# Performance work log

Hardware: AMD Instinct MI355X
Metric: run time of the kernel (lower is better)

Reference implementation:

```python
import jax, jax.numpy as jnp
import numpy as np

E = 768   # embed_size
H = 64    # head_embed_size
B = 8
T = 4096  # == ctx_size


def setup_inputs() -> dict:
    key = jax.random.key(0)
    k1, k2, k3, k4 = jax.random.split(key, 4)
    inputs = jax.random.normal(k1, (B, T, E), dtype=jnp.float32)
    # Linear weights stored as (E, H) so projection is x @ W
    scale = 1.0 / np.sqrt(E)
    Wq = jax.random.uniform(k2, (E, H), dtype=jnp.float32, minval=-scale, maxval=scale)
    Wk = jax.random.uniform(k3, (E, H), dtype=jnp.float32, minval=-scale, maxval=scale)
    Wv = jax.random.uniform(k4, (E, H), dtype=jnp.float32, minval=-scale, maxval=scale)
    return {"inputs": inputs, "Wq": Wq, "Wk": Wk, "Wv": Wv}


def reference(inputs, Wq, Wk, Wv):
    Tlen = inputs.shape[1]
    q = inputs @ Wq  # (B,T,H)
    k = inputs @ Wk  # (B,T,H)
    v = inputs @ Wv  # (B,T,H)
    # NOTE: original module does NOT scale by 1/sqrt(H) — faithful reproduction.
    scores = jnp.einsum('bqh,bkh->bqk', q, k)  # (B,T,T)
    causal = jnp.tril(jnp.ones((Tlen, Tlen), dtype=bool))
    scores = jnp.where(causal, scores, -jnp.inf)
    attn = jax.nn.softmax(scores, axis=-1)
    # dropout=0 -> identity
    out = jnp.einsum('bqk,bkh->bqh', attn, v)  # (B,T,H)
    return out
```

## Files before the change

kernel.cpp:

```cpp
#include <hip/hip_runtime.h>
#include <hip/hip_bf16.h>

#define E_DIM 768
#define H_DIM 64
#define B_SZ 8
#define T_SZ 4096
#define BT (B_SZ * T_SZ)

typedef __attribute__((ext_vector_type(8))) short short8;
typedef __attribute__((ext_vector_type(4))) short bf16x4;
typedef __attribute__((ext_vector_type(4))) float floatx4;

#define RAWBAR() __asm__ volatile("s_waitcnt lgkmcnt(0)\n\ts_barrier" ::: "memory")

static __device__ __forceinline__ unsigned short bf1(float a) {
    __hip_bfloat16 h = __float2bfloat16(a);
    unsigned short u; __builtin_memcpy(&u, &h, 2); return u;
}
static __device__ __forceinline__ unsigned int pk2(float a, float b) {
    __hip_bfloat162 h = __float22bfloat162_rn(float2{a, b});
    unsigned int u; __builtin_memcpy(&u, &h, 4); return u;
}

__global__ __launch_bounds__(256) void prep_w(
    const float* __restrict__ Wq, const float* __restrict__ Wk,
    const float* __restrict__ Wv, unsigned short* __restrict__ Wt)
{
    __shared__ float Ls[64][65];
    const int nt = blockIdx.x;
    const int kc = blockIdx.y;
    const float* __restrict__ W = (nt == 0) ? Wq : (nt == 1) ? Wk : Wv;
    const float scl = (nt == 0) ? 1.44269504088896f : 1.0f;
    const int t = threadIdx.x;
    const int k0 = kc * 64;

#pragma unroll
    for (int it = 0; it < 16; ++it) {
        const int kk = (t >> 6) + it * 4;
        Ls[kk][t & 63] = W[(size_t)(k0 + kk) * H_DIM + (t & 63)];
    }
    __syncthreads();

#pragma unroll
    for (int it = 0; it < 4; ++it) {
        const int nl = (t >> 4) + it * 16;
        const int kl = (t & 15) * 4;
        unsigned int u[2];
        u[0] = pk2(Ls[kl + 0][nl] * scl, Ls[kl + 1][nl] * scl);
        u[1] = pk2(Ls[kl + 2][nl] * scl, Ls[kl + 3][nl] * scl);
        *(uint2*)(Wt + (size_t)(nt * 64 + nl) * E_DIM + k0 + kl) = *(uint2*)u;
    }
}

__global__ __launch_bounds__(768) void proj_mfma(
    const float* __restrict__ X, const unsigned short* __restrict__ Wt,
    unsigned short* __restrict__ Qb, unsigned short* __restrict__ Kb,
    unsigned short* __restrict__ Vtb)
{
    __shared__ unsigned short Xs[2][16][776];

    const int tid  = threadIdx.x;
    const int wave = tid >> 6, lane = tid & 63;
    const int row  = lane & 15, quad = lane >> 4;
    const int m0   = blockIdx.x * 128;

    short8 bfr[24];
    {
        const unsigned short* wp = Wt + (size_t)(wave * 16 + row) * E_DIM + quad * 8;
#pragma unroll
        for (int ks = 0; ks < 24; ++ks) bfr[ks] = *(const short8*)(wp + ks * 32);
    }

    const int srow = tid & 15;
    const int sc   = tid >> 4;
    const float* __restrict__ xbase = X + (size_t)(m0 + srow) * E_DIM + sc * 16;

    float4 fx[4];
#define LDX(mt)                                                               \
    {                                                                         \
        const float* p = xbase + (size_t)(mt) * 16 * E_DIM;                   \
        fx[0] = *(const float4*)(p);     fx[1] = *(const float4*)(p + 4);     \
        fx[2] = *(const float4*)(p + 8); fx[3] = *(const float4*)(p + 12);    \
    }
#define STX(buf)                                                              \
    {                                                                         \
        unsigned int tmp[8];                                                  \
        tmp[0] = pk2(fx[0].x, fx[0].y); tmp[1] = pk2(fx[0].z, fx[0].w);       \
        tmp[2] = pk2(fx[1].x, fx[1].y); tmp[3] = pk2(fx[1].z, fx[1].w);       \
        tmp[4] = pk2(fx[2].x, fx[2].y); tmp[5] = pk2(fx[2].z, fx[2].w);       \
        tmp[6] = pk2(fx[3].x, fx[3].y); tmp[7] = pk2(fx[3].z, fx[3].w);       \
        *(int4*)&Xs[buf][srow][sc * 16]     = *(int4*)&tmp[0];                \
        *(int4*)&Xs[buf][srow][sc * 16 + 8] = *(int4*)&tmp[4];                \
    }

    LDX(0); STX(0); LDX(1);
    RAWBAR();

    const int g  = wave >> 2;
    const int h  = (wave & 3) * 16 + row;
    unsigned short* __restrict__ OQK = (g == 0) ? Qb : Kb;
    const int bb = m0 >> 12;

    int cur = 0;
    for (int mt = 0; mt < 8; ++mt) {
        if (mt < 7) STX(cur ^ 1);
        if (mt < 6) LDX(mt + 2);

        floatx4 a0 = (floatx4)0.0f, a1 = (floatx4)0.0f;
        floatx4 a2 = (floatx4)0.0f, a3 = (floatx4)0.0f;
#pragma unroll
        for (int ks = 0; ks < 6; ++ks) {
            const short8 f0 = *(const short8*)&Xs[cur][row][(ks * 4 + 0) * 32 + quad * 8];
            const short8 f1 = *(const short8*)&Xs[cur][row][(ks * 4 + 1) * 32 + quad * 8];
            const short8 f2 = *(const short8*)&Xs[cur][row][(ks * 4 + 2) * 32 + quad * 8];
            const short8 f3 = *(const short8*)&Xs[cur][row][(ks * 4 + 3) * 32 + quad * 8];
            a0 = __builtin_amdgcn_mfma_f32_16x16x32_bf16(f0, bfr[ks * 4 + 0], a0, 0, 0, 0);
            a1 = __builtin_amdgcn_mfma_f32_16x16x32_bf16(f1, bfr[ks * 4 + 1], a1, 0, 0, 0);
            a2 = __builtin_amdgcn_mfma_f32_16x16x32_bf16(f2, bfr[ks * 4 + 2], a2, 0, 0, 0);
            a3 = __builtin_amdgcn_mfma_f32_16x16x32_bf16(f3, bfr[ks * 4 + 3], a3, 0, 0, 0);
        }
        floatx4 acc;
#pragma unroll
        for (int r = 0; r < 4; ++r) acc[r] = (a0[r] + a1[r]) + (a2[r] + a3[r]);

        const int mr = m0 + mt * 16 + quad * 4;
        if (g < 2) {
#pragma unroll
            for (int r = 0; r < 4; ++r)
                OQK[(size_t)(mr + r) * H_DIM + h] = bf1(acc[r]);
        } else {
            const int t0 = mr & 4095;
            unsigned int u[2];
            u[0] = pk2(acc[0], acc[1]); u[1] = pk2(acc[2], acc[3]);
            *(uint2*)(Vtb + ((size_t)bb * H_DIM + h) * T_SZ + t0) = *(uint2*)u;
        }

        RAWBAR();
        cur ^= 1;
    }
#undef LDX
#undef STX
}

__global__ __launch_bounds__(128, 6) void attn_mfma(
    const unsigned short* __restrict__ Qb,
    const unsigned short* __restrict__ Kb,
    const unsigned short* __restrict__ Vtb,
    float* __restrict__ Opart, float* __restrict__ lpart,
    float* __restrict__ Out)
{
    __shared__ __align__(16) unsigned short Ks[32][72];
    __shared__ __align__(16) unsigned short Vs[64][40];

    const int lb = blockIdx.x;
    const int b  = lb & 7;
    const int s  = lb >> 3;
    int qq, c, m;
    if (s < 48)       { m = 6; qq = 127 - s / 6;                      c = s % 6; }
    else if (s < 168) { m = 5; const int i = s - 48;  qq = 119 - i / 5;  c = i % 5; }
    else if (s < 264) { m = 4; const int i = s - 168; qq = 95 - (i >> 2); c = i & 3; }
    else if (s < 336) { m = 3; const int i = s - 264; qq = 71 - i / 3;   c = i % 3; }
    else if (s < 384) { m = 2; const int i = s - 336; qq = 47 - (i >> 1); c = i & 1; }
    else              { m = 1; qq = 407 - s; c = 0; }
    const int ntot = qq + 1;
    const int k0t  = (c * ntot) / m;
    const int k1t  = ((c + 1) * ntot) / m;
    const int ktd  = ntot - 1;
    const int n    = k1t - k0t;
    const bool split = (m > 1);

    const int tid  = threadIdx.x;
    const int wq   = tid >> 6;
    const int lane = tid & 63;
    const int col  = lane & 15, quad = lane >> 4;

    const size_t base = (size_t)b * T_SZ * H_DIM;
    const int q0  = qq * 32;

    short8 qf0, qf1;
    {
        const unsigned short* qp = Qb + base + (size_t)(q0 + wq * 16 + col) * H_DIM + quad * 8;
        qf0 = *(const short8*)(qp);
        qf1 = *(const short8*)(qp + 32);
    }

    floatx4 o[4];
#pragma unroll
    for (int i = 0; i < 4; ++i) o[i] = (floatx4)0.0f;
    float lp = 0.0f;

    const int krow = tid >> 2, kcol = (tid & 3) * 16;
    const int vrow = tid >> 1, vcol = (tid & 1) * 16;
    const unsigned short* __restrict__ Ksrc = Kb + base + (size_t)krow * H_DIM + kcol;
    const unsigned short* __restrict__ Vsrc = Vtb + ((size_t)b * H_DIM + vrow) * T_SZ + vcol;

    int4 kr0, kr1, vr0, vr1;
#define LDKV(t)                                                          \
    {                                                                    \
        const unsigned short* kp = Ksrc + (size_t)(t) * 32 * H_DIM;      \
        kr0 = *(const int4*)kp; kr1 = *(const int4*)(kp + 8);            \
        const unsigned short* vp = Vsrc + (t) * 32;                      \
        vr0 = *(const int4*)vp; vr1 = *(const int4*)(vp + 8);            \
    }
#define STKV()                                                           \
    {                                                                    \
        *(int4*)&Ks[krow][kcol] = kr0; *(int4*)&Ks[krow][kcol + 8] = kr1; \
        *(int4*)&Vs[vrow][vcol] = vr0; *(int4*)&Vs[vrow][vcol + 8] = vr1; \
    }

    LDKV(k0t);
    STKV();
    if (n > 1) LDKV(k0t + 1);
    RAWBAR();

    for (int i = 0; i < n; ++i) {
        const int kt = k0t + i;

        floatx4 sv[2];
        __builtin_amdgcn_s_setprio(1);
#pragma unroll
        for (int j = 0; j < 2; ++j) {
            const unsigned short* kp = &Ks[j * 16 + col][quad * 8];
            floatx4 a = (floatx4)0.0f;
            a = __builtin_amdgcn_mfma_f32_16x16x32_bf16(*(const short8*)(kp),      qf0, a, 0, 0, 0);
            a = __builtin_amdgcn_mfma_f32_16x16x32_bf16(*(const short8*)(kp + 32), qf1, a, 0, 0, 0);
            sv[j] = a;
        }
        __builtin_amdgcn_s_setprio(0);

        if (kt == ktd) {
            const int qg = q0 + wq * 16 + col;
#pragma unroll
            for (int j = 0; j < 2; ++j) {
                const int kb0 = kt * 32 + j * 16 + quad * 4;
#pragma unroll
                for (int r = 0; r < 4; ++r)
                    if (kb0 + r > qg) sv[j][r] = -1e30f;
            }
        }

        bf16x4 pa[2];
#pragma unroll
        for (int j = 0; j < 2; ++j) {
            float p0 = exp2f(sv[j][0]);
            float p1 = exp2f(sv[j][1]);
            float p2 = exp2f(sv[j][2]);
            float p3 = exp2f(sv[j][3]);
            lp += (p0 + p1) + (p2 + p3);
            unsigned int u0, u1;
            __asm__("v_cvt_pk_bf16_f32 %0, %1, %2" : "=v"(u0) : "v"(p0), "v"(p1));
            __asm__("v_cvt_pk_bf16_f32 %0, %1, %2" : "=v"(u1) : "v"(p2), "v"(p3));
            union { unsigned int u[2]; bf16x4 v; } pu;
            pu.u[0] = u0; pu.u[1] = u1;
            pa[j] = pu.v;
        }

        __builtin_amdgcn_s_setprio(1);
#pragma unroll
        for (int d = 0; d < 4; ++d) {
#pragma unroll
            for (int j = 0; j < 2; ++j) {
                const bf16x4 vb = *(const bf16x4*)(&Vs[d * 16 + col][j * 16 + quad * 4]);
                o[d] = __builtin_amdgcn_mfma_f32_16x16x16bf16_1k(pa[j], vb, o[d], 0, 0, 0);
            }
        }
        __builtin_amdgcn_s_setprio(0);

        RAWBAR();
        if (i + 1 < n) {
            STKV();
            if (i + 2 < n) LDKV(kt + 2);
        }
        RAWBAR();
    }

    lp += __shfl_xor(lp, 16);
    lp += __shfl_xor(lp, 32);
    float lr[4];
#pragma unroll
    for (int r = 0; r < 4; ++r) lr[r] = __shfl(lp, quad * 4 + r);

    if (!split) {
        float* op = Out + base + (size_t)(q0 + wq * 16 + quad * 4) * H_DIM;
#pragma unroll
        for (int r = 0; r < 4; ++r) {
            const float inv = 1.0f / lr[r];
#pragma unroll
            for (int d = 0; d < 4; ++d)
                op[(size_t)r * H_DIM + d * 16 + col] = o[d][r] * inv;
        }
    } else {
        const int pidx = (b * 128 + qq) * 6 + c;
        float* op = Opart + ((size_t)pidx * 32 + wq * 16 + quad * 4) * 64;
#pragma unroll
        for (int r = 0; r < 4; ++r)
#pragma unroll
            for (int d = 0; d < 4; ++d)
                op[(size_t)r * 64 + d * 16 + col] = o[d][r];
        if (quad == 0) lpart[pidx * 32 + wq * 16 + col] = lp;
    }
#undef LDKV
#undef STKV
}

__global__ __launch_bounds__(256) void attn_combine(
    const float* __restrict__ Opart, const float* __restrict__ lpart,
    float* __restrict__ Out)
{
    const int qq  = 24 + blockIdx.x;
    const int b   = blockIdx.y;
    const int m   = (qq + 24) / 24;
    const int tid = threadIdx.x;
    const int orow = tid >> 3;
    const int d0   = (tid & 7) * 8;
    const int p0   = (b * 128 + qq) * 6;

    float4 a0 = {0.f, 0.f, 0.f, 0.f}, a1 = {0.f, 0.f, 0.f, 0.f};
    float l = 0.0f;
    for (int j = 0; j < m; ++j) {
        const float* P = Opart + ((size_t)(p0 + j) * 32 + orow) * 64 + d0;
        const float4 b0 = *(const float4*)(P);
        const float4 b1 = *(const float4*)(P + 4);
        a0.x += b0.x; a0.y += b0.y; a0.z += b0.z; a0.w += b0.w;
        a1.x += b1.x; a1.y += b1.y; a1.z += b1.z; a1.w += b1.w;
        l += lpart[(p0 + j) * 32 + orow];
    }
    const float inv = 1.0f / l;
    a0.x *= inv; a0.y *= inv; a0.z *= inv; a0.w *= inv;
    a1.x *= inv; a1.y *= inv; a1.z *= inv; a1.w *= inv;

    float* op = Out + ((size_t)b * T_SZ + qq * 32 + orow) * H_DIM + d0;
    *(float4*)(op)     = a0;
    *(float4*)(op + 4) = a1;
}

extern "C" void kernel_launch(void* const* d_in, const int* in_sizes, int n_in,
                              void* d_out, int out_size, void* d_ws, size_t ws_size,
                              hipStream_t stream) {
    const float* X  = (const float*)d_in[0];
    const float* Wq = (const float*)d_in[1];
    const float* Wk = (const float*)d_in[2];
    const float* Wv = (const float*)d_in[3];

    unsigned short* Wt  = (unsigned short*)d_ws;
    unsigned short* Qb  = Wt + (size_t)192 * E_DIM;
    unsigned short* Kb  = Qb + (size_t)BT * H_DIM;
    unsigned short* Vtb = Kb + (size_t)BT * H_DIM;
    float* Opart = (float*)(Vtb + (size_t)BT * H_DIM);
    float* lpart = Opart + (size_t)6144 * 32 * 64;

    prep_w<<<dim3(3, 12), 256, 0, stream>>>(Wq, Wk, Wv, Wt);
    proj_mfma<<<256, 768, 0, stream>>>(X, Wt, Qb, Kb, Vtb);
    attn_mfma<<<3264, 128, 0, stream>>>(Qb, Kb, Vtb, Opart, lpart, (float*)d_out);
    attn_combine<<<dim3(104, 8), 256, 0, stream>>>(Opart, lpart, (float*)d_out);
}
```

Before: 222.8 us.

## Store K/V in MFMA fragment order and run LDS-free per-wave attention

The projection kernel now writes K and V directly in a pre-swizzled fragment layout, so each lane of the attention kernel can load its MFMA operands straight from global memory with contiguous 16-byte loads. Shared memory staging and barriers are removed. Each wave now handles 32 query rows independently, with register double-buffered K prefetch over 64-key steps. PV uses the 16x16x32 instruction, and the split-K schedule is rebalanced up to 8 chunks. The cost is more register pressure, and K/V are no longer shared across waves through LDS, so L2 traffic rises.

```diff
diff --git a/kernel.cpp b/kernel.cpp
--- a/kernel.cpp
+++ b/kernel.cpp
@@ -8,7 +8,6 @@
 #define BT (B_SZ * T_SZ)
 
 typedef __attribute__((ext_vector_type(8))) short short8;
-typedef __attribute__((ext_vector_type(4))) short bf16x4;
 typedef __attribute__((ext_vector_type(4))) float floatx4;
 
 #define RAWBAR() __asm__ volatile("s_waitcnt lgkmcnt(0)\n\ts_barrier" ::: "memory")
@@ -54,8 +53,8 @@
 
 __global__ __launch_bounds__(768) void proj_mfma(
     const float* __restrict__ X, const unsigned short* __restrict__ Wt,
-    unsigned short* __restrict__ Qb, unsigned short* __restrict__ Kb,
-    unsigned short* __restrict__ Vtb)
+    unsigned short* __restrict__ Qb, unsigned short* __restrict__ KFp,
+    unsigned short* __restrict__ VFp)
 {
     __shared__ unsigned short Xs[2][16][776];
 
@@ -98,7 +97,6 @@
 
     const int g  = wave >> 2;
     const int h  = (wave & 3) * 16 + row;
-    unsigned short* __restrict__ OQK = (g == 0) ? Qb : Kb;
     const int bb = m0 >> 12;
 
     int cur = 0;
@@ -124,15 +122,33 @@
         for (int r = 0; r < 4; ++r) acc[r] = (a0[r] + a1[r]) + (a2[r] + a3[r]);
 
         const int mr = m0 + mt * 16 + quad * 4;
-        if (g < 2) {
+        const int tl = mr & 4095;
+        if (g == 0) {
 #pragma unroll
             for (int r = 0; r < 4; ++r)
-                OQK[(size_t)(mr + r) * H_DIM + h] = bf1(acc[r]);
+                Qb[(size_t)(mr + r) * H_DIM + h] = bf1(acc[r]);
+        } else if (g == 1) {
+            const int kt = tl >> 6, kk = tl & 63;
+            const int j  = kk >> 5, rr = kk & 31;
+            const int gd = (rr >> 2) & 1;
+            const int C  = (rr >> 3) * 4;
+            const int qd = (h >> 3) & 3, fd = h >> 5, ed = h & 7;
+            unsigned short* kf = KFp +
+                ((((size_t)(bb * 64 + kt) * 2 + j) * 2 + gd) * 2 + fd) * 512 +
+                (qd * 16 + C) * 8 + ed;
+#pragma unroll
+            for (int r = 0; r < 4; ++r) kf[r * 8] = bf1(acc[r]);
         } else {
-            const int t0 = mr & 4095;
+            const int kt = tl >> 6, kk = tl & 63;
+            const int j  = kk >> 5, rr = kk & 31;
+            const int qv = rr >> 3, E = rr & 7;
+            const int d  = h >> 4, cv = h & 15;
             unsigned int u[2];
             u[0] = pk2(acc[0], acc[1]); u[1] = pk2(acc[2], acc[3]);
-            *(uint2*)(Vtb + ((size_t)bb * H_DIM + h) * T_SZ + t0) = *(uint2*)u;
+            unsigned short* vf = VFp +
+                (((size_t)(bb * 64 + kt) * 2 + j) * 4 + d) * 512 +
+                (qv * 16 + cv) * 8 + E;
+            *(uint2*)vf = *(uint2*)u;
         }
 
         RAWBAR();
@@ -142,183 +158,214 @@
 #undef STX
 }
 
-__global__ __launch_bounds__(128, 6) void attn_mfma(
+__global__ __launch_bounds__(256, 4) void attn_mfma(
     const unsigned short* __restrict__ Qb,
-    const unsigned short* __restrict__ Kb,
-    const unsigned short* __restrict__ Vtb,
+    const unsigned short* __restrict__ KF,
+    const unsigned short* __restrict__ VF,
     float* __restrict__ Opart, float* __restrict__ lpart,
     float* __restrict__ Out)
 {
-    __shared__ __align__(16) unsigned short Ks[32][72];
-    __shared__ __align__(16) unsigned short Vs[64][40];
-
     const int lb = blockIdx.x;
     const int b  = lb & 7;
-    const int s  = lb >> 3;
+    const int w  = threadIdx.x >> 6;
+    const int s  = (lb >> 3) * 4 + w;
     int qq, c, m;
-    if (s < 48)       { m = 6; qq = 127 - s / 6;                      c = s % 6; }
-    else if (s < 168) { m = 5; const int i = s - 48;  qq = 119 - i / 5;  c = i % 5; }
-    else if (s < 264) { m = 4; const int i = s - 168; qq = 95 - (i >> 2); c = i & 3; }
-    else if (s < 336) { m = 3; const int i = s - 264; qq = 71 - i / 3;   c = i % 3; }
-    else if (s < 384) { m = 2; const int i = s - 336; qq = 47 - (i >> 1); c = i & 1; }
-    else              { m = 1; qq = 407 - s; c = 0; }
-    const int ntot = qq + 1;
+    if (s < 128)      { m = 8; qq = 112 + (s >> 3);                  c = s & 7; }
+    else if (s < 240) { m = 7; const int i = s - 128; qq = 96 + i / 7; c = i % 7; }
+    else if (s < 336) { m = 6; const int i = s - 240; qq = 80 + i / 6; c = i % 6; }
+    else if (s < 416) { m = 5; const int i = s - 336; qq = 64 + i / 5; c = i % 5; }
+    else if (s < 480) { m = 4; const int i = s - 416; qq = 48 + (i >> 2); c = i & 3; }
+    else if (s < 528) { m = 3; const int i = s - 480; qq = 32 + i / 3; c = i % 3; }
+    else if (s < 560) { m = 2; const int i = s - 528; qq = 16 + (i >> 1); c = i & 1; }
+    else              { m = 1; qq = s - 560; c = 0; }
+    const int ntot = (qq >> 1) + 1;
     const int k0t  = (c * ntot) / m;
     const int k1t  = ((c + 1) * ntot) / m;
     const int ktd  = ntot - 1;
-    const int n    = k1t - k0t;
+    const int ns   = (k1t - k0t) * 2;
     const bool split = (m > 1);
 
-    const int tid  = threadIdx.x;
-    const int wq   = tid >> 6;
-    const int lane = tid & 63;
+    const int lane = threadIdx.x & 63;
     const int col  = lane & 15, quad = lane >> 4;
-
     const size_t base = (size_t)b * T_SZ * H_DIM;
-    const int q0  = qq * 32;
-
-    short8 qf0, qf1;
+    const int q0 = qq * 32;
+
+    short8 qfA0, qfA1, qfB0, qfB1;
     {
-        const unsigned short* qp = Qb + base + (size_t)(q0 + wq * 16 + col) * H_DIM + quad * 8;
-        qf0 = *(const short8*)(qp);
-        qf1 = *(const short8*)(qp + 32);
-    }
-
-    floatx4 o[4];
-#pragma unroll
-    for (int i = 0; i < 4; ++i) o[i] = (floatx4)0.0f;
-    float lp = 0.0f;
-
-    const int krow = tid >> 2, kcol = (tid & 3) * 16;
-    const int vrow = tid >> 1, vcol = (tid & 1) * 16;
-    const unsigned short* __restrict__ Ksrc = Kb + base + (size_t)krow * H_DIM + kcol;
-    const unsigned short* __restrict__ Vsrc = Vtb + ((size_t)b * H_DIM + vrow) * T_SZ + vcol;
-
-    int4 kr0, kr1, vr0, vr1;
-#define LDKV(t)                                                          \
-    {                                                                    \
-        const unsigned short* kp = Ksrc + (size_t)(t) * 32 * H_DIM;      \
-        kr0 = *(const int4*)kp; kr1 = *(const int4*)(kp + 8);            \
-        const unsigned short* vp = Vsrc + (t) * 32;                      \
-        vr0 = *(const int4*)vp; vr1 = *(const int4*)(vp + 8);            \
-    }
-#define STKV()                                                           \
-    {                                                                    \
-        *(int4*)&Ks[krow][kcol] = kr0; *(int4*)&Ks[krow][kcol + 8] = kr1; \
-        *(int4*)&Vs[vrow][vcol] = vr0; *(int4*)&Vs[vrow][vcol + 8] = vr1; \
-    }
-
-    LDKV(k0t);
-    STKV();
-    if (n > 1) LDKV(k0t + 1);
-    RAWBAR();
-
-    for (int i = 0; i < n; ++i) {
-        const int kt = k0t + i;
-
-        floatx4 sv[2];
-        __builtin_amdgcn_s_setprio(1);
-#pragma unroll
-        for (int j = 0; j < 2; ++j) {
-            const unsigned short* kp = &Ks[j * 16 + col][quad * 8];
-            floatx4 a = (floatx4)0.0f;
-            a = __builtin_amdgcn_mfma_f32_16x16x32_bf16(*(const short8*)(kp),      qf0, a, 0, 0, 0);
-            a = __builtin_amdgcn_mfma_f32_16x16x32_bf16(*(const short8*)(kp + 32), qf1, a, 0, 0, 0);
-            sv[j] = a;
-        }
-        __builtin_amdgcn_s_setprio(0);
-
-        if (kt == ktd) {
-            const int qg = q0 + wq * 16 + col;
-#pragma unroll
-            for (int j = 0; j < 2; ++j) {
-                const int kb0 = kt * 32 + j * 16 + quad * 4;
-#pragma unroll
-                for (int r = 0; r < 4; ++r)
-                    if (kb0 + r > qg) sv[j][r] = -1e30f;
+        const unsigned short* qp = Qb + base + (size_t)(q0 + col) * H_DIM + quad * 8;
+        qfA0 = *(const short8*)(qp);
+        qfA1 = *(const short8*)(qp + 32);
+        qfB0 = *(const short8*)(qp + 16 * H_DIM);
+        qfB1 = *(const short8*)(qp + 16 * H_DIM + 32);
+    }
+
+    floatx4 oA[4], oB[4];
+#pragma unroll
+    for (int i = 0; i < 4; ++i) { oA[i] = (floatx4)0.0f; oB[i] = (floatx4)0.0f; }
+    float lpA = 0.0f, lpB = 0.0f;
+
+    const unsigned short* __restrict__ KFb = KF + (size_t)b * 64 * 4096;
+    const unsigned short* __restrict__ VFb = VF + (size_t)b * 64 * 4096;
+    const int lo = lane * 8;
+
+    short8 kP0, kP1, kP2, kP3, kQ0, kQ1, kQ2, kQ3, v0, v1, v2, v3;
+
+#define LDK(S, ss_)                                                           \
+    {                                                                         \
+        const unsigned short* kp = KFb + (size_t)(k0t * 2 + (ss_)) * 2048 + lo; \
+        k##S##0 = *(const short8*)(kp);        k##S##1 = *(const short8*)(kp + 512);  \
+        k##S##2 = *(const short8*)(kp + 1024); k##S##3 = *(const short8*)(kp + 1536); \
+    }
+#define LDV(ss_)                                                              \
+    {                                                                         \
+        const unsigned short* vp = VFb + (size_t)(k0t * 2 + (ss_)) * 2048 + lo; \
+        v0 = *(const short8*)(vp);        v1 = *(const short8*)(vp + 512);    \
+        v2 = *(const short8*)(vp + 1024); v3 = *(const short8*)(vp + 1536);   \
+    }
+#define COMP(S, ss_)                                                          \
+    {                                                                         \
+        const int dia = ((ss_) >> 1) + k0t == ktd;                            \
+        floatx4 aA0 = (floatx4)0.0f, aA1 = (floatx4)0.0f;                     \
+        __builtin_amdgcn_s_setprio(1);                                        \
+        aA0 = __builtin_amdgcn_mfma_f32_16x16x32_bf16(k##S##0, qfA0, aA0, 0, 0, 0); \
+        aA1 = __builtin_amdgcn_mfma_f32_16x16x32_bf16(k##S##2, qfA0, aA1, 0, 0, 0); \
+        aA0 = __builtin_amdgcn_mfma_f32_16x16x32_bf16(k##S##1, qfA1, aA0, 0, 0, 0); \
+        aA1 = __builtin_amdgcn_mfma_f32_16x16x32_bf16(k##S##3, qfA1, aA1, 0, 0, 0); \
+        __builtin_amdgcn_s_setprio(0);                                        \
+        if (dia) {                                                            \
+            const int kb = ktd * 64 + ((ss_) & 1) * 32 + quad * 8;            \
+            const int qgA = q0 + col;                                         \
+            _Pragma("unroll")                                                 \
+            for (int r = 0; r < 4; ++r) {                                     \
+                if (kb + r > qgA)     aA0[r] = -1e30f;                        \
+                if (kb + 4 + r > qgA) aA1[r] = -1e30f;                        \
+            }                                                                 \
+        }                                                                     \
+        const float pA0 = exp2f(aA0[0]), pA1 = exp2f(aA0[1]);                 \
+        const float pA2 = exp2f(aA0[2]), pA3 = exp2f(aA0[3]);                 \
+        const float pA4 = exp2f(aA1[0]), pA5 = exp2f(aA1[1]);                 \
+        const float pA6 = exp2f(aA1[2]), pA7 = exp2f(aA1[3]);                 \
+        lpA += ((pA0 + pA1) + (pA2 + pA3)) + ((pA4 + pA5) + (pA6 + pA7));     \
+        unsigned int uA0, uA1, uA2, uA3;                                      \
+        __asm__("v_cvt_pk_bf16_f32 %0, %1, %2" : "=v"(uA0) : "v"(pA0), "v"(pA1)); \
+        __asm__("v_cvt_pk_bf16_f32 %0, %1, %2" : "=v"(uA1) : "v"(pA2), "v"(pA3)); \
+        __asm__("v_cvt_pk_bf16_f32 %0, %1, %2" : "=v"(uA2) : "v"(pA4), "v"(pA5)); \
+        __asm__("v_cvt_pk_bf16_f32 %0, %1, %2" : "=v"(uA3) : "v"(pA6), "v"(pA7)); \
+        union { unsigned int u[4]; short8 v; } puA;                           \
+        puA.u[0] = uA0; puA.u[1] = uA1; puA.u[2] = uA2; puA.u[3] = uA3;       \
+        const short8 paA = puA.v;                                             \
+        floatx4 aB0 = (floatx4)0.0f, aB1 = (floatx4)0.0f;                     \
+        __builtin_amdgcn_s_setprio(1);                                        \
+        aB0 = __builtin_amdgcn_mfma_f32_16x16x32_bf16(k##S##0, qfB0, aB0, 0, 0, 0); \
+        aB1 = __builtin_amdgcn_mfma_f32_16x16x32_bf16(k##S##2, qfB0, aB1, 0, 0, 0); \
+        aB0 = __builtin_amdgcn_mfma_f32_16x16x32_bf16(k##S##1, qfB1, aB0, 0, 0, 0); \
+        aB1 = __builtin_amdgcn_mfma_f32_16x16x32_bf16(k##S##3, qfB1, aB1, 0, 0, 0); \
+        __builtin_amdgcn_s_setprio(0);                                        \
+        if (dia) {                                                            \
+            const int kb = ktd * 64 + ((ss_) & 1) * 32 + quad * 8;            \
+            const int qgB = q0 + 16 + col;                                    \
+            _Pragma("unroll")                                                 \
+            for (int r = 0; r < 4; ++r) {                                     \
+                if (kb + r > qgB)     aB0[r] = -1e30f;                        \
+                if (kb + 4 + r > qgB) aB1[r] = -1e30f;                        \
+            }                                                                 \
+        }                                                                     \
+        const float pB0 = exp2f(aB0[0]), pB1 = exp2f(aB0[1]);                 \
+        const float pB2 = exp2f(aB0[2]), pB3 = exp2f(aB0[3]);                 \
+        const float pB4 = exp2f(aB1[0]), pB5 = exp2f(aB1[1]);                 \
+        const float pB6 = exp2f(aB1[2]), pB7 = exp2f(aB1[3]);                 \
+        lpB += ((pB0 + pB1) + (pB2 + pB3)) + ((pB4 + pB5) + (pB6 + pB7));     \
+        unsigned int uB0, uB1, uB2, uB3;                                      \
+        __asm__("v_cvt_pk_bf16_f32 %0, %1, %2" : "=v"(uB0) : "v"(pB0), "v"(pB1)); \
+        __asm__("v_cvt_pk_bf16_f32 %0, %1, %2" : "=v"(uB1) : "v"(pB2), "v"(pB3)); \
+        __asm__("v_cvt_pk_bf16_f32 %0, %1, %2" : "=v"(uB2) : "v"(pB4), "v"(pB5)); \
+        __asm__("v_cvt_pk_bf16_f32 %0, %1, %2" : "=v"(uB3) : "v"(pB6), "v"(pB7)); \
+        union { unsigned int u[4]; short8 v; } puB;                           \
+        puB.u[0] = uB0; puB.u[1] = uB1; puB.u[2] = uB2; puB.u[3] = uB3;       \
+        const short8 paB = puB.v;                                             \
+        __builtin_amdgcn_s_setprio(1);                                        \
+        oA[0] = __builtin_amdgcn_mfma_f32_16x16x32_bf16(paA, v0, oA[0], 0, 0, 0); \
+        oB[0] = __builtin_amdgcn_mfma_f32_16x16x32_bf16(paB, v0, oB[0], 0, 0, 0); \
+        oA[1] = __builtin_amdgcn_mfma_f32_16x16x32_bf16(paA, v1, oA[1], 0, 0, 0); \
+        oB[1] = __builtin_amdgcn_mfma_f32_16x16x32_bf16(paB, v1, oB[1], 0, 0, 0); \
+        oA[2] = __builtin_amdgcn_mfma_f32_16x16x32_bf16(paA, v2, oA[2], 0, 0, 0); \
+        oB[2] = __builtin_amdgcn_mfma_f32_16x16x32_bf16(paB, v2, oB[2], 0, 0, 0); \
+        oA[3] = __builtin_amdgcn_mfma_f32_16x16x32_bf16(paA, v3, oA[3], 0, 0, 0); \
+        oB[3] = __builtin_amdgcn_mfma_f32_16x16x32_bf16(paB, v3, oB[3], 0, 0, 0); \
+        __builtin_amdgcn_s_setprio(0);                                        \
+    }
+
+    LDK(P, 0);
+    int ss = 0;
+    while (true) {
+        LDV(ss);
+        if (ss + 1 < ns) LDK(Q, ss + 1);
+        COMP(P, ss);
+        if (++ss >= ns) break;
+        LDV(ss);
+        if (ss + 1 < ns) LDK(P, ss + 1);
+        COMP(Q, ss);
+        if (++ss >= ns) break;
+    }
+#undef LDK
+#undef LDV
+#undef COMP
+
+    lpA += __shfl_xor(lpA, 16); lpA += __shfl_xor(lpA, 32);
+    lpB += __shfl_xor(lpB, 16); lpB += __shfl_xor(lpB, 32);
+    float lrA[4], lrB[4];
+#pragma unroll
+    for (int r = 0; r < 4; ++r) {
+        lrA[r] = __shfl(lpA, quad * 4 + r);
+        lrB[r] = __shfl(lpB, quad * 4 + r);
+    }
+
+    if (!split) {
+        float* opA = Out + base + (size_t)(q0 + quad * 4) * H_DIM;
+        float* opB = Out + base + (size_t)(q0 + 16 + quad * 4) * H_DIM;
+#pragma unroll
+        for (int r = 0; r < 4; ++r) {
+            const float invA = 1.0f / lrA[r], invB = 1.0f / lrB[r];
+#pragma unroll
+            for (int d = 0; d < 4; ++d) {
+                opA[(size_t)r * H_DIM + d * 16 + col] = oA[d][r] * invA;
+                opB[(size_t)r * H_DIM + d * 16 + col] = oB[d][r] * invB;
             }
         }
-
-        bf16x4 pa[2];
-#pragma unroll
-        for (int j = 0; j < 2; ++j) {
-            float p0 = exp2f(sv[j][0]);
-            float p1 = exp2f(sv[j][1]);
-            float p2 = exp2f(sv[j][2]);
-            float p3 = exp2f(sv[j][3]);
-            lp += (p0 + p1) + (p2 + p3);
-            unsigned int u0, u1;
-            __asm__("v_cvt_pk_bf16_f32 %0, %1, %2" : "=v"(u0) : "v"(p0), "v"(p1));
-            __asm__("v_cvt_pk_bf16_f32 %0, %1, %2" : "=v"(u1) : "v"(p2), "v"(p3));
-            union { unsigned int u[2]; bf16x4 v; } pu;
-            pu.u[0] = u0; pu.u[1] = u1;
-            pa[j] = pu.v;
+    } else {
+        const int pidx = (b * 128 + qq) * 8 + c;
+        float* opA = Opart + (size_t)pidx * 2048 + (quad * 4) * 64;
+        float* opB = Opart + (size_t)pidx * 2048 + (16 + quad * 4) * 64;
+#pragma unroll
+        for (int r = 0; r < 4; ++r)
+#pragma unroll
+            for (int d = 0; d < 4; ++d) {
+                opA[(size_t)r * 64 + d * 16 + col] = oA[d][r];
+                opB[(size_t)r * 64 + d * 16 + col] = oB[d][r];
+            }
+        if (quad == 0) {
+            lpart[pidx * 32 + col] = lpA;
+            lpart[pidx * 32 + 16 + col] = lpB;
         }
-
-        __builtin_amdgcn_s_setprio(1);
-#pragma unroll
-        for (int d = 0; d < 4; ++d) {
-#pragma unroll
-            for (int j = 0; j < 2; ++j) {
-                const bf16x4 vb = *(const bf16x4*)(&Vs[d * 16 + col][j * 16 + quad * 4]);
-                o[d] = __builtin_amdgcn_mfma_f32_16x16x16bf16_1k(pa[j], vb, o[d], 0, 0, 0);
-            }
-        }
-        __builtin_amdgcn_s_setprio(0);
-
-        RAWBAR();
-        if (i + 1 < n) {
-            STKV();
-            if (i + 2 < n) LDKV(kt + 2);
-        }
-        RAWBAR();
-    }
-
-    lp += __shfl_xor(lp, 16);
-    lp += __shfl_xor(lp, 32);
-    float lr[4];
-#pragma unroll
-    for (int r = 0; r < 4; ++r) lr[r] = __shfl(lp, quad * 4 + r);
-
-    if (!split) {
-        float* op = Out + base + (size_t)(q0 + wq * 16 + quad * 4) * H_DIM;
-#pragma unroll
-        for (int r = 0; r < 4; ++r) {
-            const float inv = 1.0f / lr[r];
-#pragma unroll
-            for (int d = 0; d < 4; ++d)
-                op[(size_t)r * H_DIM + d * 16 + col] = o[d][r] * inv;
-        }
-    } else {
-        const int pidx = (b * 128 + qq) * 6 + c;
-        float* op = Opart + ((size_t)pidx * 32 + wq * 16 + quad * 4) * 64;
-#pragma unroll
-        for (int r = 0; r < 4; ++r)
-#pragma unroll
-            for (int d = 0; d < 4; ++d)
-                op[(size_t)r * 64 + d * 16 + col] = o[d][r];
-        if (quad == 0) lpart[pidx * 32 + wq * 16 + col] = lp;
-    }
-#undef LDKV
-#undef STKV
+    }
 }
 
 __global__ __launch_bounds__(256) void attn_combine(
     const float* __restrict__ Opart, const float* __restrict__ lpart,
     float* __restrict__ Out)
 {
-    const int qq  = 24 + blockIdx.x;
+    const int qq  = 16 + blockIdx.x;
     const int b   = blockIdx.y;
-    const int m   = (qq + 24) / 24;
+    const int m   = ((qq >> 1) + 8) >> 3;
     const int tid = threadIdx.x;
     const int orow = tid >> 3;
     const int d0   = (tid & 7) * 8;
-    const int p0   = (b * 128 + qq) * 6;
+    const int p0   = (b * 128 + qq) * 8;
 
     float4 a0 = {0.f, 0.f, 0.f, 0.f}, a1 = {0.f, 0.f, 0.f, 0.f};
     float l = 0.0f;
     for (int j = 0; j < m; ++j) {
-        const float* P = Opart + ((size_t)(p0 + j) * 32 + orow) * 64 + d0;
+        const float* P = Opart + (size_t)(p0 + j) * 2048 + orow * 64 + d0;
         const float4 b0 = *(const float4*)(P);
         const float4 b1 = *(const float4*)(P + 4);
         a0.x += b0.x; a0.y += b0.y; a0.z += b0.z; a0.w += b0.w;
@@ -344,13 +391,13 @@
 
     unsigned short* Wt  = (unsigned short*)d_ws;
     unsigned short* Qb  = Wt + (size_t)192 * E_DIM;
-    unsigned short* Kb  = Qb + (size_t)BT * H_DIM;
-    unsigned short* Vtb = Kb + (size_t)BT * H_DIM;
-    float* Opart = (float*)(Vtb + (size_t)BT * H_DIM);
-    float* lpart = Opart + (size_t)6144 * 32 * 64;
+    unsigned short* KFp = Qb + (size_t)BT * H_DIM;
+    unsigned short* VFp = KFp + (size_t)BT * H_DIM;
+    float* Opart = (float*)(VFp + (size_t)BT * H_DIM);
+    float* lpart = Opart + (size_t)8192 * 2048;
 
     prep_w<<<dim3(3, 12), 256, 0, stream>>>(Wq, Wk, Wv, Wt);
-    proj_mfma<<<256, 768, 0, stream>>>(X, Wt, Qb, Kb, Vtb);
-    attn_mfma<<<3264, 128, 0, stream>>>(Qb, Kb, Vtb, Opart, lpart, (float*)d_out);
-    attn_combine<<<dim3(104, 8), 256, 0, stream>>>(Opart, lpart, (float*)d_out);
-}
+    proj_mfma<<<256, 768, 0, stream>>>(X, Wt, Qb, KFp, VFp);
+    attn_mfma<<<1152, 256, 0, stream>>>(Qb, KFp, VFp, Opart, lpart, (float*)d_out);
+    attn_combine<<<dim3(112, 8), 256, 0, stream>>>(Opart, lpart, (float*)d_out);
+}
```

Result: slower. 247.4 us (+11.0%).
